# Performance work log

Measured on AMD Instinct MI355X. Metric: run time of the kernel, lower is better.

Reference implementation:

```python
import jax, jax.numpy as jnp
import numpy as np
import math

B, S, D, H, F = 4, 1024, 1024, 16, 4096
DH = D // H
NEG = -1000000.0  # matches masked_fill value in MaskedSoftmax
EPS = 1e-5        # torch LayerNorm default


def layer_norm(x, g, b):
    m = jnp.mean(x, axis=-1, keepdims=True)
    v = jnp.mean((x - m) ** 2, axis=-1, keepdims=True)
    return (x - m) * jax.lax.rsqrt(v + EPS) * g + b


def mha(q_in, k_in, v_in, Wq, bq, Wk, bk, Wv, bv, Wo, bo, mask):
    # mask: broadcastable to [B, H, Sq, Sk]; True = keep
    Bq, Sq, _ = q_in.shape
    Sk = k_in.shape[1]
    Q = (q_in @ Wq + bq).reshape(Bq, Sq, H, DH).transpose(0, 2, 1, 3)
    K = (k_in @ Wk + bk).reshape(Bq, Sk, H, DH).transpose(0, 2, 1, 3)
    V = (v_in @ Wv + bv).reshape(Bq, Sk, H, DH).transpose(0, 2, 1, 3)
    scores = jnp.einsum('bhqd,bhkd->bhqk', Q, K) / math.sqrt(DH)
    scores = jnp.where(mask, scores, NEG)
    A = jax.nn.softmax(scores, axis=-1)
    out = jnp.einsum('bhqk,bhkd->bhqd', A, V)
    out = out.transpose(0, 2, 1, 3).reshape(Bq, Sq, D)
    return out @ Wo + bo


def setup_inputs() -> dict:
    key = jax.random.key(0)
    ks = jax.random.split(key, 16)
    w = lambda k, shp: (jax.random.normal(k, shp, dtype=jnp.float32) * 0.02)
    inp = {
        'X': jax.random.normal(ks[0], (B, S, D), dtype=jnp.float32),
        'enc_outputs': jax.random.normal(ks[1], (B, S, D), dtype=jnp.float32),
        'enc_valid_lens': jax.random.randint(ks[2], (B,), 1, S + 1),
        # self-attention
        'Wq1': w(ks[3], (D, D)), 'bq1': jnp.zeros((D,), jnp.float32),
        'Wk1': w(ks[4], (D, D)), 'bk1': jnp.zeros((D,), jnp.float32),
        'Wv1': w(ks[5], (D, D)), 'bv1': jnp.zeros((D,), jnp.float32),
        'Wo1': w(ks[6], (D, D)), 'bo1': jnp.zeros((D,), jnp.float32),
        'g1': jnp.ones((D,), jnp.float32), 'be1': jnp.zeros((D,), jnp.float32),
        # cross-attention
        'Wq2': w(ks[7], (D, D)), 'bq2': jnp.zeros((D,), jnp.float32),
        'Wk2': w(ks[8], (D, D)), 'bk2': jnp.zeros((D,), jnp.float32),
        'Wv2': w(ks[9], (D, D)), 'bv2': jnp.zeros((D,), jnp.float32),
        'Wo2': w(ks[10], (D, D)), 'bo2': jnp.zeros((D,), jnp.float32),
        'g2': jnp.ones((D,), jnp.float32), 'be2': jnp.zeros((D,), jnp.float32),
        # FFN
        'Wf1': w(ks[11], (D, F)), 'bf1': jnp.zeros((F,), jnp.float32),
        'Wf2': w(ks[12], (F, D)), 'bf2': jnp.zeros((D,), jnp.float32),
        'g3': jnp.ones((D,), jnp.float32), 'be3': jnp.zeros((D,), jnp.float32),
    }
    return inp


def reference(X, enc_outputs, enc_valid_lens,
              Wq1, bq1, Wk1, bk1, Wv1, bv1, Wo1, bo1, g1, be1,
              Wq2, bq2, Wk2, bk2, Wv2, bv2, Wo2, bo2, g2, be2,
              Wf1, bf1, Wf2, bf2, g3, be3):
    # training mode, first decode step: key_values = X, causal dec mask
    idx = jnp.arange(S)
    causal = (idx[None, :] <= idx[:, None])[None, None]          # [1,1,S,S]
    cross = (idx[None, :] < enc_valid_lens[:, None])[:, None, None, :]  # [B,1,1,S]

    X2 = mha(X, X, X, Wq1, bq1, Wk1, bk1, Wv1, bv1, Wo1, bo1, causal)
    Y = layer_norm(X2 + X, g1, be1)
    Y2 = mha(Y, enc_outputs, enc_outputs, Wq2, bq2, Wk2, bk2, Wv2, bv2, Wo2, bo2, cross)
    Z = layer_norm(Y2 + Y, g2, be2)
    ffn = jax.nn.relu(Z @ Wf1 + bf1) @ Wf2 + bf2
    return layer_norm(ffn + Z, g3, be3)
```

## Files before the change

### kernel.cpp

```cpp
#include <hip/hip_runtime.h>
#include <stdint.h>

typedef unsigned short u16;
typedef __bf16 bf16x8 __attribute__((ext_vector_type(8)));
typedef float f32x4 __attribute__((ext_vector_type(4)));

#define BB 4
#define SS 1024
#define DD 1024
#define HH 16
#define DHH 64
#define FF 4096
#define NEGV -1000000.0f
#define LOG2E 1.4426950408889634f

__device__ __forceinline__ u16 f2b(float f) {
    uint32_t u = __float_as_uint(f);
    u += 0x7fff + ((u >> 16) & 1);
    return (u16)(u >> 16);
}

__device__ __forceinline__ float exp2_raw(float x) {
    float r;
    asm volatile("v_exp_f32 %0, %1" : "=v"(r) : "v"(x));
    return r;
}

__device__ __forceinline__ void async16(const void* gp, void* lp) {
    auto g = reinterpret_cast<const __attribute__((address_space(1))) uint32_t*>(
        reinterpret_cast<uintptr_t>(gp));
    auto l = reinterpret_cast<__attribute__((address_space(3))) uint32_t*>(
        reinterpret_cast<uintptr_t>(lp));
    __builtin_amdgcn_global_load_lds(g, l, 16, 0, 0);
}

__global__ void cvt_bf16_kernel(const float* __restrict__ in, u16* __restrict__ out, int n4) {
    int i = blockIdx.x * blockDim.x + threadIdx.x;
    if (i >= n4) return;
    float4 v = reinterpret_cast<const float4*>(in)[i];
    ushort4 o;
    o.x = f2b(v.x); o.y = f2b(v.y); o.z = f2b(v.z); o.w = f2b(v.w);
    reinterpret_cast<ushort4*>(out)[i] = o;
}

__global__ void concat_bias_kernel(const float* __restrict__ a, const float* __restrict__ b,
                                   const float* __restrict__ c, float* __restrict__ out) {
    int i = blockIdx.x * 256 + threadIdx.x;
    float v;
    if (i < 1024) v = a[i];
    else if (i < 2048) v = b[i - 1024];
    else v = c[i - 2048];
    out[i] = v;
}

__global__ void wtrans_kernel(const float* __restrict__ W, u16* __restrict__ Wt, int K, int N) {
    __shared__ u16 t[64][68];
    int n0 = blockIdx.x * 64, k0 = blockIdx.y * 64;
    int tx = threadIdx.x & 15, ty = threadIdx.x >> 4;
#pragma unroll
    for (int rr = 0; rr < 4; ++rr) {
        int r = ty + rr * 16;
        float4 v = *reinterpret_cast<const float4*>(&W[(size_t)(k0 + r) * N + n0 + tx * 4]);
        ushort4 o;
        o.x = f2b(v.x); o.y = f2b(v.y); o.z = f2b(v.z); o.w = f2b(v.w);
        *reinterpret_cast<ushort4*>(&t[r][tx * 4]) = o;
    }
    __syncthreads();
#pragma unroll
    for (int rr = 0; rr < 4; ++rr) {
        int n = ty + rr * 16;
        ushort4 o;
        o.x = t[tx * 4 + 0][n];
        o.y = t[tx * 4 + 1][n];
        o.z = t[tx * 4 + 2][n];
        o.w = t[tx * 4 + 3][n];
        *reinterpret_cast<ushort4*>(&Wt[(size_t)(n0 + n) * K + k0 + tx * 4]) = o;
    }
}

__global__ void vtrans_kernel(const u16* __restrict__ V, int ldv, u16* __restrict__ VT) {
    __shared__ u16 t[32][33];
    int bh = blockIdx.z;
    int b = bh >> 4, h = bh & 15;
    int s0 = blockIdx.x * 32, d0 = blockIdx.y * 32;
    int tx = threadIdx.x, ty = threadIdx.y;
#pragma unroll
    for (int r = 0; r < 32; r += 8)
        t[ty + r][tx] = V[(size_t)(b * SS + s0 + ty + r) * ldv + h * DHH + d0 + tx];
    __syncthreads();
#pragma unroll
    for (int r = 0; r < 32; r += 8)
        VT[(size_t)(bh * DHH + d0 + ty + r) * SS + s0 + tx] = t[tx][ty + r];
}

template<int BM, bool OUT_BF16, bool RELU, int KSPLIT = 1>
__global__ __launch_bounds__(256, 3) void gemm_bt_kernel(
    const u16* __restrict__ A, const u16* __restrict__ Bt,
    const float* __restrict__ bias, void* __restrict__ Cv,
    int M, int N, int K, int qcols, float qscale)
{
    constexpr int MR = BM / 32;
    __shared__ __attribute__((aligned(16))) u16 As[BM][64];
    __shared__ __attribute__((aligned(16))) u16 Bs[128][64];
    const int tid = threadIdx.x;
    const int lane = tid & 63, wid = tid >> 6;
    const int wr = wid >> 1, wc = wid & 1;
    const int m0 = blockIdx.x * BM, n0 = blockIdx.y * 128;
    const int kz = (KSPLIT > 1) ? blockIdx.z : 0;
    const int Kc = K / KSPLIT;
    const int k0 = kz * Kc;
    const int arow = lane & 15;
    const int kseg = (lane >> 4) * 8;
    const int srow = lane >> 3;
    const int scol = ((lane & 7) ^ srow) * 8;
    const int rswz = (arow & 7) << 3;
    const f32x4 z4 = {0.f, 0.f, 0.f, 0.f};

    f32x4 acc[MR][4];
#pragma unroll
    for (int i = 0; i < MR; ++i)
#pragma unroll
        for (int j = 0; j < 4; ++j) acc[i][j] = z4;

    for (int kt = k0; kt < k0 + Kc; kt += 64) {
        __syncthreads();
#pragma unroll
        for (int i = 0; i < MR; ++i) {
            int ch = wid + i * 4;
            async16(&A[(size_t)(m0 + ch * 8 + srow) * K + kt + scol], &As[ch * 8][0]);
        }
#pragma unroll
        for (int i = 0; i < 4; ++i) {
            int ch = wid + i * 4;
            async16(&Bt[(size_t)(n0 + ch * 8 + srow) * K + kt + scol], &Bs[ch * 8][0]);
        }
        __syncthreads();
#pragma unroll
        for (int ks = 0; ks < 2; ++ks) {
            const int cswz = (ks * 32 + kseg) ^ rswz;
            bf16x8 af[MR], bfr[4];
#pragma unroll
            for (int mi = 0; mi < MR; ++mi)
                af[mi] = *reinterpret_cast<const bf16x8*>(&As[wr * (BM / 2) + mi * 16 + arow][cswz]);
#pragma unroll
            for (int ni = 0; ni < 4; ++ni)
                bfr[ni] = *reinterpret_cast<const bf16x8*>(&Bs[wc * 64 + ni * 16 + arow][cswz]);
#pragma unroll
            for (int mi = 0; mi < MR; ++mi)
#pragma unroll
                for (int ni = 0; ni < 4; ++ni)
                    acc[mi][ni] = __builtin_amdgcn_mfma_f32_16x16x32_bf16(af[mi], bfr[ni], acc[mi][ni], 0, 0, 0);
        }
    }
    const int rrow = (lane >> 4) * 4;
#pragma unroll
    for (int mi = 0; mi < MR; ++mi)
#pragma unroll
        for (int ni = 0; ni < 4; ++ni) {
            int col = n0 + wc * 64 + ni * 16 + arow;
            float bv = (kz == 0) ? bias[col] : 0.f;
            float sc = (col < qcols) ? qscale : 1.f;
#pragma unroll
            for (int r = 0; r < 4; ++r) {
                int row = m0 + wr * (BM / 2) + mi * 16 + rrow + r;
                float v = (acc[mi][ni][r] + bv) * sc;
                if (RELU) v = fmaxf(v, 0.f);
                if (OUT_BF16) ((u16*)Cv)[(size_t)row * N + col] = f2b(v);
                else          ((float*)Cv)[(size_t)kz * M * N + (size_t)row * N + col] = v;
            }
        }
}

__global__ __launch_bounds__(256, 2) void flash_attn_kernel(
    const u16* __restrict__ Q, int ldq, const u16* __restrict__ Kp, int ldk,
    const u16* __restrict__ VT, u16* __restrict__ O,
    const int* __restrict__ vlens, int causal)
{
    __shared__ __attribute__((aligned(16))) u16 Ks[128][64];
    __shared__ __attribute__((aligned(16))) u16 Vs[64][128];
    __shared__ __attribute__((aligned(16))) u16 Ps[128][64];
    const int tid = threadIdx.x, lane = tid & 63, wid = tid >> 6;
    const int bh = blockIdx.x;
    int qb = blockIdx.y;
    if (causal) qb = (bh & 1) ? (7 - qb) : qb;
    const int b = bh >> 4, h = bh & 15;
    const int q0 = qb * 128;
    const int a = lane & 15;
    const int g = lane >> 4;
    const int kseg = g * 8;
    const int srow = lane >> 3;
    const int scol = ((lane & 7) ^ srow) * 8;
    const int vrow = lane >> 4;
    const int vscol = ((lane & 15) ^ (wid * 4 + vrow)) * 8;
    const int rswz = (a & 7) << 3;
    const int vswz = a << 3;
    const f32x4 z4 = {0.f, 0.f, 0.f, 0.f};

    bf16x8 qf[2][2];
#pragma unroll
    for (int mi = 0; mi < 2; ++mi)
#pragma unroll
        for (int ks = 0; ks < 2; ++ks)
            qf[mi][ks] = *reinterpret_cast<const bf16x8*>(
                &Q[(size_t)(b * SS + q0 + wid * 32 + mi * 16 + a) * ldq + h * DHH + ks * 32 + kseg]);

    float m_run[2], l_run[2];
    f32x4 o[2][4];
#pragma unroll
    for (int mi = 0; mi < 2; ++mi) {
        m_run[mi] = -3e38f; l_run[mi] = 0.f;
#pragma unroll
        for (int nd = 0; nd < 4; ++nd) o[mi][nd] = z4;
    }

    int vl = causal ? SS : vlens[b];
    int ntiles = causal ? (qb + 1) : ((vl + 127) >> 7);

    for (int kt = 0; kt < ntiles; ++kt) {
        const int kv0 = kt * 128;
        __syncthreads();
#pragma unroll
        for (int i = 0; i < 4; ++i) {
            int ch = wid + i * 4;
            async16(&Kp[(size_t)(b * SS + kv0 + ch * 8 + srow) * ldk + h * DHH + scol], &Ks[ch * 8][0]);
        }
#pragma unroll
        for (int i = 0; i < 4; ++i) {
            int cv = wid + i * 4;
            async16(&VT[(size_t)(bh * DHH + cv * 4 + vrow) * SS + kv0 + vscol], &Vs[cv * 4][0]);
        }
        __syncthreads();

        f32x4 st[2][8];
#pragma unroll
        for (int mi = 0; mi < 2; ++mi)
#pragma unroll
            for (int ni = 0; ni < 8; ++ni) st[mi][ni] = z4;
        __builtin_amdgcn_s_setprio(1);
#pragma unroll
        for (int ks = 0; ks < 2; ++ks) {
            const int cswz = (ks * 32 + kseg) ^ rswz;
            bf16x8 kf[8];
#pragma unroll
            for (int ni = 0; ni < 8; ++ni)
                kf[ni] = *reinterpret_cast<const bf16x8*>(&Ks[ni * 16 + a][cswz]);
#pragma unroll
            for (int mi = 0; mi < 2; ++mi)
#pragma unroll
                for (int ni = 0; ni < 8; ++ni)
                    st[mi][ni] = __builtin_amdgcn_mfma_f32_16x16x32_bf16(kf[ni], qf[mi][ks], st[mi][ni], 0, 0, 0);
        }
        __builtin_amdgcn_s_setprio(0);

        bool domask = causal ? (kt == qb) : (kv0 + 128 > vl);
        if (domask) {
#pragma unroll
            for (int mi = 0; mi < 2; ++mi) {
                const int qg = q0 + wid * 32 + mi * 16 + a;
#pragma unroll
                for (int ni = 0; ni < 8; ++ni)
#pragma unroll
                    for (int r = 0; r < 4; ++r) {
                        int cg = kv0 + ni * 16 + 4 * g + r;
                        bool keep = causal ? (cg <= qg) : (cg < vl);
                        if (!keep) st[mi][ni][r] = NEGV;
                    }
            }
        }

        float corr[2];
        bool need[2];
#pragma unroll
        for (int mi = 0; mi < 2; ++mi) {
            float tm = -3e38f;
#pragma unroll
            for (int ni = 0; ni < 8; ++ni)
#pragma unroll
                for (int r = 0; r < 4; ++r) tm = fmaxf(tm, st[mi][ni][r]);
            tm = fmaxf(tm, __shfl_xor(tm, 16));
            tm = fmaxf(tm, __shfl_xor(tm, 32));
            need[mi] = __any(tm > m_run[mi] + 11.0f);
            if (need[mi]) {
                float nm = fmaxf(m_run[mi], tm);
                corr[mi] = exp2_raw(m_run[mi] - nm);
                m_run[mi] = nm;
            } else {
                corr[mi] = 1.f;
            }
            float nm2 = m_run[mi];
            float rs = 0.f;
#pragma unroll
            for (int ni = 0; ni < 8; ++ni)
#pragma unroll
                for (int r = 0; r < 4; ++r) {
                    float p = exp2_raw(st[mi][ni][r] - nm2);
                    st[mi][ni][r] = p;
                    rs += p;
                }
            rs += __shfl_xor(rs, 16);
            rs += __shfl_xor(rs, 32);
            l_run[mi] = l_run[mi] * corr[mi] + rs;
        }

#pragma unroll
        for (int mi = 0; mi < 2; ++mi) {
            if (need[mi]) {
#pragma unroll
                for (int r = 0; r < 4; ++r) {
                    float cr = __shfl(corr[mi], (lane & 48) + 4 * g + r);
#pragma unroll
                    for (int nd = 0; nd < 4; ++nd) o[mi][nd][r] *= cr;
                }
            }
        }

#pragma unroll
        for (int hh = 0; hh < 2; ++hh) {
#pragma unroll
            for (int mi = 0; mi < 2; ++mi)
#pragma unroll
                for (int ni4 = 0; ni4 < 4; ++ni4) {
                    int ni = hh * 4 + ni4;
                    uint2 pw;
                    pw.x = (uint32_t)f2b(st[mi][ni][0]) | ((uint32_t)f2b(st[mi][ni][1]) << 16);
                    pw.y = (uint32_t)f2b(st[mi][ni][2]) | ((uint32_t)f2b(st[mi][ni][3]) << 16);
                    int prow = wid * 32 + mi * 16 + a;
                    int pcol = (ni4 * 16 + 4 * g) ^ rswz;
                    *reinterpret_cast<uint2*>(&Ps[prow][pcol]) = pw;
                }
            __builtin_amdgcn_s_setprio(1);
#pragma unroll
            for (int kk = 0; kk < 2; ++kk) {
                const int kf_ = hh * 2 + kk;
                const int pswz = (kk * 32 + kseg) ^ rswz;
                const int cvswz = (kf_ * 32 + kseg) ^ vswz;
                bf16x8 pa[2], vb[4];
#pragma unroll
                for (int mi = 0; mi < 2; ++mi)
                    pa[mi] = *reinterpret_cast<const bf16x8*>(&Ps[wid * 32 + mi * 16 + a][pswz]);
#pragma unroll
                for (int nd = 0; nd < 4; ++nd)
                    vb[nd] = *reinterpret_cast<const bf16x8*>(&Vs[nd * 16 + a][cvswz]);
#pragma unroll
                for (int mi = 0; mi < 2; ++mi)
#pragma unroll
                    for (int nd = 0; nd < 4; ++nd)
                        o[mi][nd] = __builtin_amdgcn_mfma_f32_16x16x32_bf16(pa[mi], vb[nd], o[mi][nd], 0, 0, 0);
            }
            __builtin_amdgcn_s_setprio(0);
        }
    }

#pragma unroll
    for (int mi = 0; mi < 2; ++mi) {
        float il = 1.f / l_run[mi];
#pragma unroll
        for (int r = 0; r < 4; ++r) {
            float ilr = __shfl(il, (lane & 48) + 4 * g + r);
            int row = q0 + wid * 32 + mi * 16 + 4 * g + r;
#pragma unroll
            for (int nd = 0; nd < 4; ++nd)
                O[(size_t)(b * SS + row) * DD + h * DHH + nd * 16 + a] = f2b(o[mi][nd][r] * ilr);
        }
    }
}

__global__ void add_ln_kernel(const float* __restrict__ A, const float* __restrict__ A2,
                              const float* __restrict__ R,
                              const float* __restrict__ g, const float* __restrict__ be,
                              float* __restrict__ out32, u16* __restrict__ out16)
{
    __shared__ float red[4][2];
    const int row = blockIdx.x, tid = threadIdx.x;
    const size_t base = (size_t)row * DD;
    float4 va = *reinterpret_cast<const float4*>(A + base + tid * 4);
    float4 vb = *reinterpret_cast<const float4*>(A2 + base + tid * 4);
    float4 vr = *reinterpret_cast<const float4*>(R + base + tid * 4);
    float x0 = va.x + vb.x + vr.x, x1 = va.y + vb.y + vr.y;
    float x2 = va.z + vb.z + vr.z, x3 = va.w + vb.w + vr.w;
    float s = x0 + x1 + x2 + x3;
    float q = x0 * x0 + x1 * x1 + x2 * x2 + x3 * x3;
#pragma unroll
    for (int off = 32; off; off >>= 1) {
        s += __shfl_xor(s, off);
        q += __shfl_xor(q, off);
    }
    if ((tid & 63) == 0) { red[tid >> 6][0] = s; red[tid >> 6][1] = q; }
    __syncthreads();
    s = red[0][0] + red[1][0] + red[2][0] + red[3][0];
    q = red[0][1] + red[1][1] + red[2][1] + red[3][1];
    float mean = s * (1.f / 1024.f);
    float var = q * (1.f / 1024.f) - mean * mean;
    float rstd = rsqrtf(var + 1e-5f);
    int c = tid * 4;
    float o0 = (x0 - mean) * rstd * g[c + 0] + be[c + 0];
    float o1 = (x1 - mean) * rstd * g[c + 1] + be[c + 1];
    float o2 = (x2 - mean) * rstd * g[c + 2] + be[c + 2];
    float o3 = (x3 - mean) * rstd * g[c + 3] + be[c + 3];
    float4 ov = {o0, o1, o2, o3};
    *reinterpret_cast<float4*>(out32 + base + c) = ov;
    if (out16) {
        ushort4 hv;
        hv.x = f2b(o0); hv.y = f2b(o1); hv.z = f2b(o2); hv.w = f2b(o3);
        *reinterpret_cast<ushort4*>(out16 + base + c) = hv;
    }
}

extern "C" void kernel_launch(void* const* d_in, const int* in_sizes, int n_in,
                              void* d_out, int out_size, void* d_ws, size_t ws_size,
                              hipStream_t stream)
{
    const float* X   = (const float*)d_in[0];
    const float* ENC = (const float*)d_in[1];
    const int*   VL  = (const int*)d_in[2];
    const float* Wq1 = (const float*)d_in[3];  const float* bq1 = (const float*)d_in[4];
    const float* Wk1 = (const float*)d_in[5];  const float* bk1 = (const float*)d_in[6];
    const float* Wv1 = (const float*)d_in[7];  const float* bv1 = (const float*)d_in[8];
    const float* Wo1 = (const float*)d_in[9];  const float* bo1 = (const float*)d_in[10];
    const float* g1  = (const float*)d_in[11]; const float* be1 = (const float*)d_in[12];
    const float* Wq2 = (const float*)d_in[13]; const float* bq2 = (const float*)d_in[14];
    const float* Wk2 = (const float*)d_in[15]; const float* bk2 = (const float*)d_in[16];
    const float* Wv2 = (const float*)d_in[17]; const float* bv2 = (const float*)d_in[18];
    const float* Wo2 = (const float*)d_in[19]; const float* bo2 = (const float*)d_in[20];
    const float* g2  = (const float*)d_in[21]; const float* be2 = (const float*)d_in[22];
    const float* Wf1 = (const float*)d_in[23]; const float* bf1 = (const float*)d_in[24];
    const float* Wf2 = (const float*)d_in[25]; const float* bf2 = (const float*)d_in[26];
    const float* g3  = (const float*)d_in[27]; const float* be3 = (const float*)d_in[28];

    char* ws = (char*)d_ws;
    const size_t MB = 1024 * 1024;
    u16*   XBF  = (u16*)(ws + 0 * MB);
    u16*   ENCB = (u16*)(ws + 8 * MB);
    u16*   WT   = (u16*)(ws + 16 * MB);
    u16*   QKV  = (u16*)(ws + 24 * MB);
    u16*   HF   = (u16*)(ws + 24 * MB);
    u16*   VTb  = (u16*)(ws + 48 * MB);
    u16*   AO   = (u16*)(ws + 56 * MB);
    float* P32  = (float*)(ws + 64 * MB);
    float* Y32  = (float*)(ws + 96 * MB);
    u16*   YBF  = (u16*)(ws + 112 * MB);
    float* Z32  = (float*)(ws + 120 * MB);
    u16*   ZBF  = (u16*)(ws + 136 * MB);
    float* B1   = (float*)(ws + 144 * MB);
    float* B2   = (float*)(ws + 144 * MB + 65536);
    (void)ws_size; (void)in_sizes; (void)n_in; (void)out_size;

    const int M = BB * SS;
    const size_t MN = (size_t)M * DD;
    const float QS = 0.125f * LOG2E;

    cvt_bf16_kernel<<<M * DD / 4 / 256, 256, 0, stream>>>(X, XBF, M * DD / 4);
    cvt_bf16_kernel<<<M * DD / 4 / 256, 256, 0, stream>>>(ENC, ENCB, M * DD / 4);

    concat_bias_kernel<<<12, 256, 0, stream>>>(bq1, bk1, bv1, B1);
    wtrans_kernel<<<dim3(16, 16), 256, 0, stream>>>(Wq1, WT, DD, DD);
    wtrans_kernel<<<dim3(16, 16), 256, 0, stream>>>(Wk1, WT + 1024 * 1024, DD, DD);
    wtrans_kernel<<<dim3(16, 16), 256, 0, stream>>>(Wv1, WT + 2048 * 1024, DD, DD);
    gemm_bt_kernel<128, true, false><<<dim3(32, 24), 256, 0, stream>>>(XBF, WT, B1, QKV, M, 3072, DD, 1024, QS);
    vtrans_kernel<<<dim3(32, 2, 64), dim3(32, 8), 0, stream>>>(QKV + 2048, 3072, VTb);
    flash_attn_kernel<<<dim3(64, 8), 256, 0, stream>>>(QKV, 3072, QKV + 1024, 3072, VTb, AO, VL, 1);
    wtrans_kernel<<<dim3(16, 16), 256, 0, stream>>>(Wo1, WT, DD, DD);
    gemm_bt_kernel<128, false, false, 2><<<dim3(32, 8, 2), 256, 0, stream>>>(AO, WT, bo1, P32, M, DD, DD, 0, 1.f);
    add_ln_kernel<<<M, 256, 0, stream>>>(P32, P32 + MN, X, g1, be1, Y32, YBF);

    wtrans_kernel<<<dim3(16, 16), 256, 0, stream>>>(Wq2, WT, DD, DD);
    gemm_bt_kernel<64, true, false><<<dim3(64, 8), 256, 0, stream>>>(YBF, WT, bq2, XBF, M, DD, DD, 1024, QS);
    concat_bias_kernel<<<8, 256, 0, stream>>>(bk2, bv2, bv2, B2);
    wtrans_kernel<<<dim3(16, 16), 256, 0, stream>>>(Wk2, WT, DD, DD);
    wtrans_kernel<<<dim3(16, 16), 256, 0, stream>>>(Wv2, WT + 1024 * 1024, DD, DD);
    gemm_bt_kernel<128, true, false><<<dim3(32, 16), 256, 0, stream>>>(ENCB, WT, B2, QKV, M, 2048, DD, 0, 1.f);
    vtrans_kernel<<<dim3(32, 2, 64), dim3(32, 8), 0, stream>>>(QKV + 1024, 2048, VTb);
    flash_attn_kernel<<<dim3(64, 8), 256, 0, stream>>>(XBF, 1024, QKV, 2048, VTb, AO, VL, 0);
    wtrans_kernel<<<dim3(16, 16), 256, 0, stream>>>(Wo2, WT, DD, DD);
    gemm_bt_kernel<128, false, false, 2><<<dim3(32, 8, 2), 256, 0, stream>>>(AO, WT, bo2, P32, M, DD, DD, 0, 1.f);
    add_ln_kernel<<<M, 256, 0, stream>>>(P32, P32 + MN, Y32, g2, be2, Z32, ZBF);

    wtrans_kernel<<<dim3(64, 16), 256, 0, stream>>>(Wf1, WT, DD, FF);
    gemm_bt_kernel<128, true, true><<<dim3(32, 32), 256, 0, stream>>>(ZBF, WT, bf1, HF, M, FF, DD, 0, 1.f);
    wtrans_kernel<<<dim3(16, 64), 256, 0, stream>>>(Wf2, WT, FF, DD);
    gemm_bt_kernel<128, false, false, 2><<<dim3(32, 8, 2), 256, 0, stream>>>(HF, WT, bf2, P32, M, DD, FF, 0, 1.f);
    add_ln_kernel<<<M, 256, 0, stream>>>(P32, P32 + MN, Z32, g3, be3, (float*)d_out, nullptr);
}
```

Measured before the change: 353.9 us.

## Batch weight transposes, bf16 split-K partials, and 512-thread flash attention

The eight square weight transposes now run in one batched launch, and the FFN weight transposes are hoisted to the start into dedicated buffers, so fewer kernels are launched. The split-K GEMM partials are written as bf16 instead of fp32 and summed in add_ln, halving that intermediate traffic at the cost of extra rounding error. Flash attention now uses 8 waves of 16 query rows each instead of 4 waves of 32, which raises parallelism but halves the reuse of each K/V fragment per wave. The bias concatenation buffers now live in the output buffer.

Measured after the change: 326.5 us. 7.7% less time.

```diff
diff --git a/kernel.cpp b/kernel.cpp
--- a/kernel.cpp
+++ b/kernel.cpp
@@ -19,6 +19,9 @@
     u += 0x7fff + ((u >> 16) & 1);
     return (u16)(u >> 16);
 }
+__device__ __forceinline__ float b2f(u16 u) {
+    return __uint_as_float(((uint32_t)u) << 16);
+}
 
 __device__ __forceinline__ float exp2_raw(float x) {
     float r;
@@ -51,6 +54,34 @@
     else if (i < 2048) v = b[i - 1024];
     else v = c[i - 2048];
     out[i] = v;
+}
+
+struct W8 { const float* p[8]; };
+__global__ void wtrans8_kernel(W8 wp, u16* __restrict__ dst) {
+    __shared__ u16 t[64][68];
+    const float* W = wp.p[blockIdx.z];
+    u16* Wt = dst + (size_t)blockIdx.z * 1024 * 1024;
+    int n0 = blockIdx.x * 64, k0 = blockIdx.y * 64;
+    int tx = threadIdx.x & 15, ty = threadIdx.x >> 4;
+#pragma unroll
+    for (int rr = 0; rr < 4; ++rr) {
+        int r = ty + rr * 16;
+        float4 v = *reinterpret_cast<const float4*>(&W[(size_t)(k0 + r) * 1024 + n0 + tx * 4]);
+        ushort4 o;
+        o.x = f2b(v.x); o.y = f2b(v.y); o.z = f2b(v.z); o.w = f2b(v.w);
+        *reinterpret_cast<ushort4*>(&t[r][tx * 4]) = o;
+    }
+    __syncthreads();
+#pragma unroll
+    for (int rr = 0; rr < 4; ++rr) {
+        int n = ty + rr * 16;
+        ushort4 o;
+        o.x = t[tx * 4 + 0][n];
+        o.y = t[tx * 4 + 1][n];
+        o.z = t[tx * 4 + 2][n];
+        o.w = t[tx * 4 + 3][n];
+        *reinterpret_cast<ushort4*>(&Wt[(size_t)(n0 + n) * 1024 + k0 + tx * 4]) = o;
+    }
 }
 
 __global__ void wtrans_kernel(const float* __restrict__ W, u16* __restrict__ Wt, int K, int N) {
@@ -165,13 +196,14 @@
                 int row = m0 + wr * (BM / 2) + mi * 16 + rrow + r;
                 float v = (acc[mi][ni][r] + bv) * sc;
                 if (RELU) v = fmaxf(v, 0.f);
-                if (OUT_BF16) ((u16*)Cv)[(size_t)row * N + col] = f2b(v);
-                else          ((float*)Cv)[(size_t)kz * M * N + (size_t)row * N + col] = v;
+                size_t idx = (size_t)kz * M * N + (size_t)row * N + col;
+                if (OUT_BF16) ((u16*)Cv)[idx] = f2b(v);
+                else          ((float*)Cv)[idx] = v;
             }
         }
 }
 
-__global__ __launch_bounds__(256, 2) void flash_attn_kernel(
+__global__ __launch_bounds__(512, 4) void flash_attn_kernel(
     const u16* __restrict__ Q, int ldq, const u16* __restrict__ Kp, int ldk,
     const u16* __restrict__ VT, u16* __restrict__ O,
     const int* __restrict__ vlens, int causal)
@@ -191,27 +223,20 @@
     const int srow = lane >> 3;
     const int scol = ((lane & 7) ^ srow) * 8;
     const int vrow = lane >> 4;
-    const int vscol = ((lane & 15) ^ (wid * 4 + vrow)) * 8;
     const int rswz = (a & 7) << 3;
     const int vswz = a << 3;
     const f32x4 z4 = {0.f, 0.f, 0.f, 0.f};
 
-    bf16x8 qf[2][2];
-#pragma unroll
-    for (int mi = 0; mi < 2; ++mi)
-#pragma unroll
-        for (int ks = 0; ks < 2; ++ks)
-            qf[mi][ks] = *reinterpret_cast<const bf16x8*>(
-                &Q[(size_t)(b * SS + q0 + wid * 32 + mi * 16 + a) * ldq + h * DHH + ks * 32 + kseg]);
-
-    float m_run[2], l_run[2];
-    f32x4 o[2][4];
-#pragma unroll
-    for (int mi = 0; mi < 2; ++mi) {
-        m_run[mi] = -3e38f; l_run[mi] = 0.f;
-#pragma unroll
-        for (int nd = 0; nd < 4; ++nd) o[mi][nd] = z4;
-    }
+    bf16x8 qf[2];
+#pragma unroll
+    for (int ks = 0; ks < 2; ++ks)
+        qf[ks] = *reinterpret_cast<const bf16x8*>(
+            &Q[(size_t)(b * SS + q0 + wid * 16 + a) * ldq + h * DHH + ks * 32 + kseg]);
+
+    float m_run = -3e38f, l_run = 0.f;
+    f32x4 o[4];
+#pragma unroll
+    for (int nd = 0; nd < 4; ++nd) o[nd] = z4;
 
     int vl = causal ? SS : vlens[b];
     int ntiles = causal ? (qb + 1) : ((vl + 127) >> 7);
@@ -220,22 +245,18 @@
         const int kv0 = kt * 128;
         __syncthreads();
 #pragma unroll
-        for (int i = 0; i < 4; ++i) {
-            int ch = wid + i * 4;
+        for (int i = 0; i < 2; ++i) {
+            int ch = wid + i * 8;
             async16(&Kp[(size_t)(b * SS + kv0 + ch * 8 + srow) * ldk + h * DHH + scol], &Ks[ch * 8][0]);
-        }
-#pragma unroll
-        for (int i = 0; i < 4; ++i) {
-            int cv = wid + i * 4;
-            async16(&VT[(size_t)(bh * DHH + cv * 4 + vrow) * SS + kv0 + vscol], &Vs[cv * 4][0]);
+            int cv = wid + i * 8;
+            int vs = (cv * 4 + vrow) & 15;
+            async16(&VT[(size_t)(bh * DHH + cv * 4 + vrow) * SS + kv0 + ((lane & 15) ^ vs) * 8], &Vs[cv * 4][0]);
         }
         __syncthreads();
 
-        f32x4 st[2][8];
-#pragma unroll
-        for (int mi = 0; mi < 2; ++mi)
-#pragma unroll
-            for (int ni = 0; ni < 8; ++ni) st[mi][ni] = z4;
+        f32x4 st[8];
+#pragma unroll
+        for (int ni = 0; ni < 8; ++ni) st[ni] = z4;
         __builtin_amdgcn_s_setprio(1);
 #pragma unroll
         for (int ks = 0; ks < 2; ++ks) {
@@ -245,127 +266,103 @@
             for (int ni = 0; ni < 8; ++ni)
                 kf[ni] = *reinterpret_cast<const bf16x8*>(&Ks[ni * 16 + a][cswz]);
 #pragma unroll
-            for (int mi = 0; mi < 2; ++mi)
-#pragma unroll
-                for (int ni = 0; ni < 8; ++ni)
-                    st[mi][ni] = __builtin_amdgcn_mfma_f32_16x16x32_bf16(kf[ni], qf[mi][ks], st[mi][ni], 0, 0, 0);
+            for (int ni = 0; ni < 8; ++ni)
+                st[ni] = __builtin_amdgcn_mfma_f32_16x16x32_bf16(kf[ni], qf[ks], st[ni], 0, 0, 0);
         }
         __builtin_amdgcn_s_setprio(0);
 
         bool domask = causal ? (kt == qb) : (kv0 + 128 > vl);
         if (domask) {
-#pragma unroll
-            for (int mi = 0; mi < 2; ++mi) {
-                const int qg = q0 + wid * 32 + mi * 16 + a;
-#pragma unroll
-                for (int ni = 0; ni < 8; ++ni)
-#pragma unroll
-                    for (int r = 0; r < 4; ++r) {
-                        int cg = kv0 + ni * 16 + 4 * g + r;
-                        bool keep = causal ? (cg <= qg) : (cg < vl);
-                        if (!keep) st[mi][ni][r] = NEGV;
-                    }
+            const int qg = q0 + wid * 16 + a;
+#pragma unroll
+            for (int ni = 0; ni < 8; ++ni)
+#pragma unroll
+                for (int r = 0; r < 4; ++r) {
+                    int cg = kv0 + ni * 16 + 4 * g + r;
+                    bool keep = causal ? (cg <= qg) : (cg < vl);
+                    if (!keep) st[ni][r] = NEGV;
+                }
+        }
+
+        float tm = -3e38f;
+#pragma unroll
+        for (int ni = 0; ni < 8; ++ni)
+#pragma unroll
+            for (int r = 0; r < 4; ++r) tm = fmaxf(tm, st[ni][r]);
+        tm = fmaxf(tm, __shfl_xor(tm, 16));
+        tm = fmaxf(tm, __shfl_xor(tm, 32));
+        bool need = __any(tm > m_run + 11.0f);
+        float corr = 1.f;
+        if (need) {
+            float nm = fmaxf(m_run, tm);
+            corr = exp2_raw(m_run - nm);
+            m_run = nm;
+        }
+        float rs = 0.f;
+#pragma unroll
+        for (int ni = 0; ni < 8; ++ni)
+#pragma unroll
+            for (int r = 0; r < 4; ++r) {
+                float p = exp2_raw(st[ni][r] - m_run);
+                st[ni][r] = p;
+                rs += p;
             }
-        }
-
-        float corr[2];
-        bool need[2];
-#pragma unroll
-        for (int mi = 0; mi < 2; ++mi) {
-            float tm = -3e38f;
-#pragma unroll
-            for (int ni = 0; ni < 8; ++ni)
-#pragma unroll
-                for (int r = 0; r < 4; ++r) tm = fmaxf(tm, st[mi][ni][r]);
-            tm = fmaxf(tm, __shfl_xor(tm, 16));
-            tm = fmaxf(tm, __shfl_xor(tm, 32));
-            need[mi] = __any(tm > m_run[mi] + 11.0f);
-            if (need[mi]) {
-                float nm = fmaxf(m_run[mi], tm);
-                corr[mi] = exp2_raw(m_run[mi] - nm);
-                m_run[mi] = nm;
-            } else {
-                corr[mi] = 1.f;
+        rs += __shfl_xor(rs, 16);
+        rs += __shfl_xor(rs, 32);
+        l_run = l_run * corr + rs;
+
+        if (need) {
+#pragma unroll
+            for (int r = 0; r < 4; ++r) {
+                float cr = __shfl(corr, (lane & 48) + 4 * g + r);
+#pragma unroll
+                for (int nd = 0; nd < 4; ++nd) o[nd][r] *= cr;
             }
-            float nm2 = m_run[mi];
-            float rs = 0.f;
-#pragma unroll
-            for (int ni = 0; ni < 8; ++ni)
-#pragma unroll
-                for (int r = 0; r < 4; ++r) {
-                    float p = exp2_raw(st[mi][ni][r] - nm2);
-                    st[mi][ni][r] = p;
-                    rs += p;
-                }
-            rs += __shfl_xor(rs, 16);
-            rs += __shfl_xor(rs, 32);
-            l_run[mi] = l_run[mi] * corr[mi] + rs;
-        }
-
-#pragma unroll
-        for (int mi = 0; mi < 2; ++mi) {
-            if (need[mi]) {
-#pragma unroll
-                for (int r = 0; r < 4; ++r) {
-                    float cr = __shfl(corr[mi], (lane & 48) + 4 * g + r);
-#pragma unroll
-                    for (int nd = 0; nd < 4; ++nd) o[mi][nd][r] *= cr;
-                }
+        }
+
+#pragma unroll
+        for (int hh = 0; hh < 2; ++hh) {
+#pragma unroll
+            for (int ni4 = 0; ni4 < 4; ++ni4) {
+                int ni = hh * 4 + ni4;
+                uint2 pw;
+                pw.x = (uint32_t)f2b(st[ni][0]) | ((uint32_t)f2b(st[ni][1]) << 16);
+                pw.y = (uint32_t)f2b(st[ni][2]) | ((uint32_t)f2b(st[ni][3]) << 16);
+                int prow = wid * 16 + a;
+                int pcol = (ni4 * 16 + 4 * g) ^ rswz;
+                *reinterpret_cast<uint2*>(&Ps[prow][pcol]) = pw;
             }
-        }
-
-#pragma unroll
-        for (int hh = 0; hh < 2; ++hh) {
-#pragma unroll
-            for (int mi = 0; mi < 2; ++mi)
-#pragma unroll
-                for (int ni4 = 0; ni4 < 4; ++ni4) {
-                    int ni = hh * 4 + ni4;
-                    uint2 pw;
-                    pw.x = (uint32_t)f2b(st[mi][ni][0]) | ((uint32_t)f2b(st[mi][ni][1]) << 16);
-                    pw.y = (uint32_t)f2b(st[mi][ni][2]) | ((uint32_t)f2b(st[mi][ni][3]) << 16);
-                    int prow = wid * 32 + mi * 16 + a;
-                    int pcol = (ni4 * 16 + 4 * g) ^ rswz;
-                    *reinterpret_cast<uint2*>(&Ps[prow][pcol]) = pw;
-                }
             __builtin_amdgcn_s_setprio(1);
 #pragma unroll
             for (int kk = 0; kk < 2; ++kk) {
                 const int kf_ = hh * 2 + kk;
                 const int pswz = (kk * 32 + kseg) ^ rswz;
                 const int cvswz = (kf_ * 32 + kseg) ^ vswz;
-                bf16x8 pa[2], vb[4];
-#pragma unroll
-                for (int mi = 0; mi < 2; ++mi)
-                    pa[mi] = *reinterpret_cast<const bf16x8*>(&Ps[wid * 32 + mi * 16 + a][pswz]);
+                bf16x8 pa, vb[4];
+                pa = *reinterpret_cast<const bf16x8*>(&Ps[wid * 16 + a][pswz]);
 #pragma unroll
                 for (int nd = 0; nd < 4; ++nd)
                     vb[nd] = *reinterpret_cast<const bf16x8*>(&Vs[nd * 16 + a][cvswz]);
 #pragma unroll
-                for (int mi = 0; mi < 2; ++mi)
-#pragma unroll
-                    for (int nd = 0; nd < 4; ++nd)
-                        o[mi][nd] = __builtin_amdgcn_mfma_f32_16x16x32_bf16(pa[mi], vb[nd], o[mi][nd], 0, 0, 0);
+                for (int nd = 0; nd < 4; ++nd)
+                    o[nd] = __builtin_amdgcn_mfma_f32_16x16x32_bf16(pa, vb[nd], o[nd], 0, 0, 0);
             }
             __builtin_amdgcn_s_setprio(0);
         }
     }
 
-#pragma unroll
-    for (int mi = 0; mi < 2; ++mi) {
-        float il = 1.f / l_run[mi];
-#pragma unroll
-        for (int r = 0; r < 4; ++r) {
-            float ilr = __shfl(il, (lane & 48) + 4 * g + r);
-            int row = q0 + wid * 32 + mi * 16 + 4 * g + r;
-#pragma unroll
-            for (int nd = 0; nd < 4; ++nd)
-                O[(size_t)(b * SS + row) * DD + h * DHH + nd * 16 + a] = f2b(o[mi][nd][r] * ilr);
-        }
-    }
-}
-
-__global__ void add_ln_kernel(const float* __restrict__ A, const float* __restrict__ A2,
+    float il = 1.f / l_run;
+#pragma unroll
+    for (int r = 0; r < 4; ++r) {
+        float ilr = __shfl(il, (lane & 48) + 4 * g + r);
+        int row = q0 + wid * 16 + 4 * g + r;
+#pragma unroll
+        for (int nd = 0; nd < 4; ++nd)
+            O[(size_t)(b * SS + row) * DD + h * DHH + nd * 16 + a] = f2b(o[nd][r] * ilr);
+    }
+}
+
+__global__ void add_ln_kernel(const u16* __restrict__ A, const u16* __restrict__ A2,
                               const float* __restrict__ R,
                               const float* __restrict__ g, const float* __restrict__ be,
                               float* __restrict__ out32, u16* __restrict__ out16)
@@ -373,11 +370,11 @@
     __shared__ float red[4][2];
     const int row = blockIdx.x, tid = threadIdx.x;
     const size_t base = (size_t)row * DD;
-    float4 va = *reinterpret_cast<const float4*>(A + base + tid * 4);
-    float4 vb = *reinterpret_cast<const float4*>(A2 + base + tid * 4);
+    ushort4 ua = *reinterpret_cast<const ushort4*>(A + base + tid * 4);
+    ushort4 ub = *reinterpret_cast<const ushort4*>(A2 + base + tid * 4);
     float4 vr = *reinterpret_cast<const float4*>(R + base + tid * 4);
-    float x0 = va.x + vb.x + vr.x, x1 = va.y + vb.y + vr.y;
-    float x2 = va.z + vb.z + vr.z, x3 = va.w + vb.w + vr.w;
+    float x0 = b2f(ua.x) + b2f(ub.x) + vr.x, x1 = b2f(ua.y) + b2f(ub.y) + vr.y;
+    float x2 = b2f(ua.z) + b2f(ub.z) + vr.z, x3 = b2f(ua.w) + b2f(ub.w) + vr.w;
     float s = x0 + x1 + x2 + x3;
     float q = x0 * x0 + x1 * x1 + x2 * x2 + x3 * x3;
 #pragma unroll
@@ -431,18 +428,20 @@
     const size_t MB = 1024 * 1024;
     u16*   XBF  = (u16*)(ws + 0 * MB);
     u16*   ENCB = (u16*)(ws + 8 * MB);
-    u16*   WT   = (u16*)(ws + 16 * MB);
-    u16*   QKV  = (u16*)(ws + 24 * MB);
-    u16*   HF   = (u16*)(ws + 24 * MB);
-    u16*   VTb  = (u16*)(ws + 48 * MB);
-    u16*   AO   = (u16*)(ws + 56 * MB);
-    float* P32  = (float*)(ws + 64 * MB);
-    float* Y32  = (float*)(ws + 96 * MB);
-    u16*   YBF  = (u16*)(ws + 112 * MB);
-    float* Z32  = (float*)(ws + 120 * MB);
-    u16*   ZBF  = (u16*)(ws + 136 * MB);
-    float* B1   = (float*)(ws + 144 * MB);
-    float* B2   = (float*)(ws + 144 * MB + 65536);
+    u16*   WTsq = (u16*)(ws + 16 * MB);
+    u16*   WTf1 = (u16*)(ws + 32 * MB);
+    u16*   WTf2 = (u16*)(ws + 40 * MB);
+    u16*   QKV  = (u16*)(ws + 48 * MB);
+    u16*   HF   = (u16*)(ws + 48 * MB);
+    u16*   VTb  = (u16*)(ws + 80 * MB);
+    u16*   AO   = (u16*)(ws + 88 * MB);
+    u16*   P16  = (u16*)(ws + 96 * MB);
+    float* Y32  = (float*)(ws + 112 * MB);
+    u16*   YBF  = (u16*)(ws + 128 * MB);
+    float* Z32  = (float*)(ws + 136 * MB);
+    u16*   ZBF  = (u16*)(ws + 152 * MB);
+    float* B1 = (float*)d_out;
+    float* B2 = (float*)d_out + 4096;
     (void)ws_size; (void)in_sizes; (void)n_in; (void)out_size;
 
     const int M = BB * SS;
@@ -451,33 +450,27 @@
 
     cvt_bf16_kernel<<<M * DD / 4 / 256, 256, 0, stream>>>(X, XBF, M * DD / 4);
     cvt_bf16_kernel<<<M * DD / 4 / 256, 256, 0, stream>>>(ENC, ENCB, M * DD / 4);
-
     concat_bias_kernel<<<12, 256, 0, stream>>>(bq1, bk1, bv1, B1);
-    wtrans_kernel<<<dim3(16, 16), 256, 0, stream>>>(Wq1, WT, DD, DD);
-    wtrans_kernel<<<dim3(16, 16), 256, 0, stream>>>(Wk1, WT + 1024 * 1024, DD, DD);
-    wtrans_kernel<<<dim3(16, 16), 256, 0, stream>>>(Wv1, WT + 2048 * 1024, DD, DD);
-    gemm_bt_kernel<128, true, false><<<dim3(32, 24), 256, 0, stream>>>(XBF, WT, B1, QKV, M, 3072, DD, 1024, QS);
+    concat_bias_kernel<<<8, 256, 0, stream>>>(bk2, bv2, bv2, B2);
+    W8 w8 = {{Wq1, Wk1, Wv1, Wo1, Wq2, Wk2, Wv2, Wo2}};
+    wtrans8_kernel<<<dim3(16, 16, 8), 256, 0, stream>>>(w8, WTsq);
+    wtrans_kernel<<<dim3(64, 16), 256, 0, stream>>>(Wf1, WTf1, DD, FF);
+    wtrans_kernel<<<dim3(16, 64), 256, 0, stream>>>(Wf2, WTf2, FF, DD);
+
+    gemm_bt_kernel<128, true, false><<<dim3(32, 24), 256, 0, stream>>>(XBF, WTsq, B1, QKV, M, 3072, DD, 1024, QS);
     vtrans_kernel<<<dim3(32, 2, 64), dim3(32, 8), 0, stream>>>(QKV + 2048, 3072, VTb);
-    flash_attn_kernel<<<dim3(64, 8), 256, 0, stream>>>(QKV, 3072, QKV + 1024, 3072, VTb, AO, VL, 1);
-    wtrans_kernel<<<dim3(16, 16), 256, 0, stream>>>(Wo1, WT, DD, DD);
-    gemm_bt_kernel<128, false, false, 2><<<dim3(32, 8, 2), 256, 0, stream>>>(AO, WT, bo1, P32, M, DD, DD, 0, 1.f);
-    add_ln_kernel<<<M, 256, 0, stream>>>(P32, P32 + MN, X, g1, be1, Y32, YBF);
-
-    wtrans_kernel<<<dim3(16, 16), 256, 0, stream>>>(Wq2, WT, DD, DD);
-    gemm_bt_kernel<64, true, false><<<dim3(64, 8), 256, 0, stream>>>(YBF, WT, bq2, XBF, M, DD, DD, 1024, QS);
-    concat_bias_kernel<<<8, 256, 0, stream>>>(bk2, bv2, bv2, B2);
-    wtrans_kernel<<<dim3(16, 16), 256, 0, stream>>>(Wk2, WT, DD, DD);
-    wtrans_kernel<<<dim3(16, 16), 256, 0, stream>>>(Wv2, WT + 1024 * 1024, DD, DD);
-    gemm_bt_kernel<128, true, false><<<dim3(32, 16), 256, 0, stream>>>(ENCB, WT, B2, QKV, M, 2048, DD, 0, 1.f);
+    flash_attn_kernel<<<dim3(64, 8), 512, 0, stream>>>(QKV, 3072, QKV + 1024, 3072, VTb, AO, VL, 1);
+    gemm_bt_kernel<128, true, false, 2><<<dim3(32, 8, 2), 256, 0, stream>>>(AO, WTsq + 3u * 1024 * 1024, bo1, P16, M, DD, DD, 0, 1.f);
+    add_ln_kernel<<<M, 256, 0, stream>>>(P16, P16 + MN, X, g1, be1, Y32, YBF);
+
+    gemm_bt_kernel<64, true, false><<<dim3(64, 8), 256, 0, stream>>>(YBF, WTsq + 4u * 1024 * 1024, bq2, XBF, M, DD, DD, 1024, QS);
+    gemm_bt_kernel<128, true, false><<<dim3(32, 16), 256, 0, stream>>>(ENCB, WTsq + 5u * 1024 * 1024, B2, QKV, M, 2048, DD, 0, 1.f);
     vtrans_kernel<<<dim3(32, 2, 64), dim3(32, 8), 0, stream>>>(QKV + 1024, 2048, VTb);
-    flash_attn_kernel<<<dim3(64, 8), 256, 0, stream>>>(XBF, 1024, QKV, 2048, VTb, AO, VL, 0);
-    wtrans_kernel<<<dim3(16, 16), 256, 0, stream>>>(Wo2, WT, DD, DD);
-    gemm_bt_kernel<128, false, false, 2><<<dim3(32, 8, 2), 256, 0, stream>>>(AO, WT, bo2, P32, M, DD, DD, 0, 1.f);
-    add_ln_kernel<<<M, 256, 0, stream>>>(P32, P32 + MN, Y32, g2, be2, Z32, ZBF);
-
-    wtrans_kernel<<<dim3(64, 16), 256, 0, stream>>>(Wf1, WT, DD, FF);
-    gemm_bt_kernel<128, true, true><<<dim3(32, 32), 256, 0, stream>>>(ZBF, WT, bf1, HF, M, FF, DD, 0, 1.f);
-    wtrans_kernel<<<dim3(16, 64), 256, 0, stream>>>(Wf2, WT, FF, DD);
-    gemm_bt_kernel<128, false, false, 2><<<dim3(32, 8, 2), 256, 0, stream>>>(HF, WT, bf2, P32, M, DD, FF, 0, 1.f);
-    add_ln_kernel<<<M, 256, 0, stream>>>(P32, P32 + MN, Z32, g3, be3, (float*)d_out, nullptr);
-}
+    flash_attn_kernel<<<dim3(64, 8), 512, 0, stream>>>(XBF, 1024, QKV, 2048, VTb, AO, VL, 0);
+    gemm_bt_kernel<128, true, false, 2><<<dim3(32, 8, 2), 256, 0, stream>>>(AO, WTsq + 7u * 1024 * 1024, bo2, P16, M, DD, DD, 0, 1.f);
+    add_ln_kernel<<<M, 256, 0, stream>>>(P16, P16 + MN, Y32, g2, be2, Z32, ZBF);
+
+    gemm_bt_kernel<128, true, true><<<dim3(32, 32), 256, 0, stream>>>(ZBF, WTf1, bf1, HF, M, FF, DD, 0, 1.f);
+    gemm_bt_kernel<128, true, false, 2><<<dim3(32, 8, 2), 256, 0, stream>>>(HF, WTf2, bf2, P16, M, DD, FF, 0, 1.f);
+    add_ln_kernel<<<M, 256, 0, stream>>>(P16, P16 + MN, Z32, g3, be3, (float*)d_out, nullptr);
+}
```
